# Performance work log

Measured on AMD Instinct MI355X. Metric: run time of the kernel, lower is better.

The kernel has to match this reference:

```python
import jax, jax.numpy as jnp
import numpy as np

NVEC = (3, 3, 4, 25, 25, 8)  # MultiDiscrete sub-action sizes; sum = 68


def _segmented_log_softmax(x, axis=-1):
    """log_softmax applied independently within each sub-action segment along last dim."""
    parts = []
    s = 0
    for n in NVEC:
        parts.append(jax.nn.log_softmax(x[..., s:s + n], axis=axis))
        s += n
    return jnp.concatenate(parts, axis=-1)


def setup_inputs() -> dict:
    key = jax.random.key(0)
    k1, k2 = jax.random.split(key)
    A = int(sum(NVEC))
    W = 524288
    current_action = jax.random.normal(k1, (A,), dtype=jnp.float32)
    previous_actions = jax.random.normal(k2, (W, A), dtype=jnp.float32)
    return {"current_action": current_action, "previous_actions": previous_actions}


def reference(current_action, previous_actions):
    W = previous_actions.shape[0]
    # logits=True path: segmented log_softmax on both inputs
    x = _segmented_log_softmax(current_action)          # [A] log-probs (KLDiv 'input')
    t = _segmented_log_softmax(previous_actions)        # [W, A] log-probs (KLDiv 'target', log_target=True)
    # KLDivLoss(log_target=True): exp(t) * (t - x); reduction='batchmean' on a 1D
    # slice of length n_j divides by n_j (input.size(0)).
    inv_n = jnp.asarray(np.repeat(1.0 / np.asarray(NVEC, dtype=np.float32), NVEC))  # [A]
    loss = jnp.sum(jnp.exp(t) * (t - x[None, :]) * inv_n[None, :])
    return loss / W
```

## Files before the change

kernel.cpp:

```cpp
#include <hip/hip_runtime.h>


namespace {
constexpr int kA = 68;
constexpr int kF4 = 17;
constexpr int kNSeg = 6;
constexpr int kOff[kNSeg + 1] = {0, 3, 6, 10, 35, 60, 68};
constexpr float kInvN[kNSeg] = {1.f/3.f, 1.f/3.f, 1.f/4.f, 1.f/25.f, 1.f/25.f, 1.f/8.f};
constexpr int kTileRows = 128;
constexpr int kTileF4 = kTileRows * kF4;
constexpr int kChunks = kTileF4 / 64;
constexpr int kGrid = 512;
}

__global__ __launch_bounds__(256) void asl_kernel(
    const float* __restrict__ cur,
    const float* __restrict__ prev,
    float* __restrict__ out,
    int W, int numTiles, float invW)
{
    __shared__ float4 buf[2][kTileF4];
    __shared__ float xs[kA];
    __shared__ float wsum[4];

    const int tid  = threadIdx.x;
    const int wave = tid >> 6;
    const int lane = tid & 63;
    const int swzl = lane ^ ((lane >> 3) & 7);

    if (tid < kNSeg) {
        const int o = kOff[tid], e = kOff[tid + 1];
        float s = 0.f;
        for (int j = o; j < e; ++j) s += __expf(cur[j]);
        const float L = __logf(s);
        for (int j = o; j < e; ++j) xs[j] = cur[j] - L;
    }

    const float4* prev4 = (const float4*)prev;
    const long totalF4 = (long)W * kF4;

    auto stage = [&](int b, int t) {
        const long base = (long)t * kTileF4;
        #pragma unroll
        for (int k = 0; k < 9; ++k) {
            const int ch = wave + 4 * k;
            if (ch >= kChunks) break;
            long g = base + ch * 64 + swzl;
            if (g >= totalF4) g = totalF4 - 1;
            __builtin_amdgcn_global_load_lds(
                (const __attribute__((address_space(1))) void*)(prev4 + g),
                (__attribute__((address_space(3))) void*)(&buf[b][ch * 64]),
                16, 0, 0);
        }
    };

    const int half = tid >> 7;
    const int r    = tid & 127;
    const int c0   = half * 8;
    float acc = 0.f;
    int buf_i = 0;
    int tile  = blockIdx.x;
    if (tile < numTiles) stage(0, tile);

    for (; tile < numTiles; tile += kGrid) {
        __syncthreads();
        const int nt = tile + kGrid;
        if (nt < numTiles) stage(buf_i ^ 1, nt);

        float vloc[36];
        {
            const float4* bp = buf[buf_i];
            const int qb = r * kF4 + c0;
            #pragma unroll
            for (int k = 0; k < 9; ++k) {
                const int q  = qb + k;
                const int qs = q ^ ((q >> 3) & 7);
                ((float4*)vloc)[k] = bp[qs];
            }
        }

        const int rowg = tile * kTileRows + r;
        if (rowg < W) {
            if (half == 0) {
                #pragma unroll
                for (int sg = 0; sg < 4; ++sg) {
                    const int o = kOff[sg], n = kOff[sg + 1] - kOff[sg];
                    float s = 0.f, d = 0.f;
                    #pragma unroll
                    for (int j = 0; j < n; ++j) {
                        const float x = vloc[o + j];
                        const float e = __expf(x);
                        s += e;
                        d = fmaf(e, x - xs[o + j], d);
                    }
                    acc += kInvN[sg] * (d * __builtin_amdgcn_rcpf(s) - __logf(s));
                }
            } else {
                #pragma unroll
                for (int sg = 4; sg < 6; ++sg) {
                    const int o = kOff[sg], n = kOff[sg + 1] - kOff[sg];
                    float s = 0.f, d = 0.f;
                    #pragma unroll
                    for (int j = 0; j < n; ++j) {
                        const float x = vloc[o - 32 + j];
                        const float e = __expf(x);
                        s += e;
                        d = fmaf(e, x - xs[o + j], d);
                    }
                    acc += kInvN[sg] * (d * __builtin_amdgcn_rcpf(s) - __logf(s));
                }
            }
        }
        buf_i ^= 1;
    }

    acc *= invW;
    #pragma unroll
    for (int o2 = 32; o2 > 0; o2 >>= 1) acc += __shfl_down(acc, o2, 64);
    if (lane == 0) wsum[wave] = acc;
    __syncthreads();
    if (tid == 0) atomicAdd(out, wsum[0] + wsum[1] + wsum[2] + wsum[3]);
}

extern "C" void kernel_launch(void* const* d_in, const int* in_sizes, int n_in,
                              void* d_out, int out_size, void* d_ws, size_t ws_size,
                              hipStream_t stream) {
    const float* cur  = (const float*)d_in[0];
    const float* prev = (const float*)d_in[1];
    float* out = (float*)d_out;

    const int W = in_sizes[1] / kA;
    const int numTiles = (W + kTileRows - 1) / kTileRows;

    hipMemsetAsync(out, 0, sizeof(float), stream);
    asl_kernel<<<kGrid, 256, 0, stream>>>(cur, prev, out, W, numTiles, 1.0f / (float)W);
}
```

Measured before the change: 205.2 us.

## Split segments across waves with smaller tiles and larger grid

```diff
diff --git a/kernel.cpp b/kernel.cpp
--- a/kernel.cpp
+++ b/kernel.cpp
@@ -6,11 +6,10 @@
 constexpr int kF4 = 17;
 constexpr int kNSeg = 6;
 constexpr int kOff[kNSeg + 1] = {0, 3, 6, 10, 35, 60, 68};
-constexpr float kInvN[kNSeg] = {1.f/3.f, 1.f/3.f, 1.f/4.f, 1.f/25.f, 1.f/25.f, 1.f/8.f};
-constexpr int kTileRows = 128;
+constexpr int kTileRows = 64;
 constexpr int kTileF4 = kTileRows * kF4;
 constexpr int kChunks = kTileF4 / 64;
-constexpr int kGrid = 512;
+constexpr int kGrid = 1024;
 }
 
 __global__ __launch_bounds__(256) void asl_kernel(
@@ -28,21 +27,13 @@
     const int lane = tid & 63;
     const int swzl = lane ^ ((lane >> 3) & 7);
 
-    if (tid < kNSeg) {
-        const int o = kOff[tid], e = kOff[tid + 1];
-        float s = 0.f;
-        for (int j = o; j < e; ++j) s += __expf(cur[j]);
-        const float L = __logf(s);
-        for (int j = o; j < e; ++j) xs[j] = cur[j] - L;
-    }
-
     const float4* prev4 = (const float4*)prev;
     const long totalF4 = (long)W * kF4;
 
     auto stage = [&](int b, int t) {
         const long base = (long)t * kTileF4;
         #pragma unroll
-        for (int k = 0; k < 9; ++k) {
+        for (int k = 0; k < 5; ++k) {
             const int ch = wave + 4 * k;
             if (ch >= kChunks) break;
             long g = base + ch * 64 + swzl;
@@ -54,61 +45,93 @@
         }
     };
 
-    const int half = tid >> 7;
-    const int r    = tid & 127;
-    const int c0   = half * 8;
-    float acc = 0.f;
     int buf_i = 0;
     int tile  = blockIdx.x;
     if (tile < numTiles) stage(0, tile);
+
+    if (tid < kNSeg) {
+        const int o = kOff[tid], e = kOff[tid + 1];
+        float s = 0.f;
+        for (int j = o; j < e; ++j) s += __expf(cur[j]);
+        const float L = __logf(s);
+        for (int j = o; j < e; ++j) xs[j] = cur[j] - L;
+    }
+
+    const int r = lane;
+    float acc = 0.f;
 
     for (; tile < numTiles; tile += kGrid) {
         __syncthreads();
         const int nt = tile + kGrid;
         if (nt < numTiles) stage(buf_i ^ 1, nt);
 
-        float vloc[36];
-        {
-            const float4* bp = buf[buf_i];
-            const int qb = r * kF4 + c0;
-            #pragma unroll
-            for (int k = 0; k < 9; ++k) {
-                const int q  = qb + k;
-                const int qs = q ^ ((q >> 3) & 7);
-                ((float4*)vloc)[k] = bp[qs];
-            }
-        }
+        const float4* bp = buf[buf_i];
+        const int qb = r * kF4;
+        const bool ok = (tile * kTileRows + r) < W;
 
-        const int rowg = tile * kTileRows + r;
-        if (rowg < W) {
-            if (half == 0) {
+        auto ldg = [&](int c) {
+            const int q = qb + c;
+            return bp[q ^ ((q >> 3) & 7)];
+        };
+
+        if (ok) {
+            if (wave == 0) {
+                float v[12];
                 #pragma unroll
-                for (int sg = 0; sg < 4; ++sg) {
+                for (int k = 0; k < 3; ++k) ((float4*)v)[k] = ldg(k);
+                #pragma unroll
+                for (int sg = 0; sg < 3; ++sg) {
                     const int o = kOff[sg], n = kOff[sg + 1] - kOff[sg];
                     float s = 0.f, d = 0.f;
                     #pragma unroll
                     for (int j = 0; j < n; ++j) {
-                        const float x = vloc[o + j];
+                        const float x = v[o + j];
                         const float e = __expf(x);
                         s += e;
                         d = fmaf(e, x - xs[o + j], d);
                     }
-                    acc += kInvN[sg] * (d * __builtin_amdgcn_rcpf(s) - __logf(s));
+                    const float invN = (sg == 2) ? 0.25f : (1.f / 3.f);
+                    acc += invN * (d * __builtin_amdgcn_rcpf(s) - __logf(s));
                 }
+            } else if (wave == 1) {
+                float v[28];
+                #pragma unroll
+                for (int k = 0; k < 7; ++k) ((float4*)v)[k] = ldg(2 + k);
+                float s = 0.f, d = 0.f;
+                #pragma unroll
+                for (int j = 0; j < 25; ++j) {
+                    const float x = v[2 + j];
+                    const float e = __expf(x);
+                    s += e;
+                    d = fmaf(e, x - xs[10 + j], d);
+                }
+                acc += (1.f / 25.f) * (d * __builtin_amdgcn_rcpf(s) - __logf(s));
+            } else if (wave == 2) {
+                float v[28];
+                #pragma unroll
+                for (int k = 0; k < 7; ++k) ((float4*)v)[k] = ldg(8 + k);
+                float s = 0.f, d = 0.f;
+                #pragma unroll
+                for (int j = 0; j < 25; ++j) {
+                    const float x = v[3 + j];
+                    const float e = __expf(x);
+                    s += e;
+                    d = fmaf(e, x - xs[35 + j], d);
+                }
+                acc += (1.f / 25.f) * (d * __builtin_amdgcn_rcpf(s) - __logf(s));
             } else {
+                float v[8];
                 #pragma unroll
-                for (int sg = 4; sg < 6; ++sg) {
-                    const int o = kOff[sg], n = kOff[sg + 1] - kOff[sg];
-                    float s = 0.f, d = 0.f;
-                    #pragma unroll
-                    for (int j = 0; j < n; ++j) {
-                        const float x = vloc[o - 32 + j];
-                        const float e = __expf(x);
-                        s += e;
-                        d = fmaf(e, x - xs[o + j], d);
-                    }
-                    acc += kInvN[sg] * (d * __builtin_amdgcn_rcpf(s) - __logf(s));
+                for (int k = 0; k < 2; ++k) ((float4*)v)[k] = ldg(15 + k);
+                float s = 0.f, d = 0.f;
+                #pragma unroll
+                for (int j = 0; j < 8; ++j) {
+                    const float x = v[j];
+                    const float e = __expf(x);
+                    s += e;
+                    d = fmaf(e, x - xs[60 + j], d);
                 }
+                acc += 0.125f * (d * __builtin_amdgcn_rcpf(s) - __logf(s));
             }
         }
         buf_i ^= 1;
```

Measured after the change: 209.3 us. Within noise of the previous version (+2.0%).
